# Kernel tuning notes

Hardware: AMD Instinct MI355X
Metric: run time of the kernel (lower is better)

Reference implementation:

```python
import jax, jax.numpy as jnp
import numpy as np

D_IN = 1024
D_OUT = 1024
NUM_HEADS = 16
HEAD_DIM = D_OUT // NUM_HEADS


def setup_inputs() -> dict:
    key = jax.random.key(0)
    kx, kq, kk, kv, ko = jax.random.split(key, 5)
    s = 1.0 / np.sqrt(D_IN)
    return {
        "x": jax.random.normal(kx, (1, 4096, D_IN), dtype=jnp.float32),
        "Wq": jax.random.normal(kq, (D_IN, D_OUT), dtype=jnp.float32) * s,
        "Wk": jax.random.normal(kk, (D_IN, D_OUT), dtype=jnp.float32) * s,
        "Wv": jax.random.normal(kv, (D_IN, D_OUT), dtype=jnp.float32) * s,
        "Wo": jax.random.normal(ko, (D_OUT, D_OUT), dtype=jnp.float32) * s,
    }


def reference(x, Wq, Wk, Wv, Wo):
    b, s, _ = x.shape
    # project and split heads: [b, h, s, d]
    def split_heads(t):
        return t.reshape(b, s, NUM_HEADS, HEAD_DIM).transpose(0, 2, 1, 3)
    Q = split_heads(x @ Wq)
    K = split_heads(x @ Wk)
    V = split_heads(x @ Wv)
    scores = jnp.einsum("bhqd,bhkd->bhqk", Q, K) / jnp.sqrt(jnp.float32(HEAD_DIM))
    causal = jnp.triu(jnp.ones((s, s), dtype=bool), k=1)  # True above diagonal
    scores = jnp.where(causal, -jnp.inf, scores)
    probs = jax.nn.softmax(scores, axis=-1)
    out = jnp.einsum("bhqk,bhkd->bhqd", probs, V)
    out = out.transpose(0, 2, 1, 3).reshape(b, s, D_OUT)
    return out @ Wo
```

## Files before the change

### kernel.cpp

```cpp
#include <hip/hip_runtime.h>
#include <cstdint>

#define S_LEN 4096
#define D_MODEL 1024
#define NHEAD 16
#define HDIM 64

typedef __bf16 bf16_t;
typedef __bf16 bf16x8 __attribute__((ext_vector_type(8)));
typedef __bf16 bf16x4 __attribute__((ext_vector_type(4)));
typedef float floatx4 __attribute__((ext_vector_type(4)));

#define QSCALE 0.18033688011112042f

__device__ __forceinline__ void lds_cp16(void* lds, const void* g) {
    __builtin_amdgcn_global_load_lds(
        (const __attribute__((address_space(1))) unsigned int*)g,
        (__attribute__((address_space(3))) unsigned int*)lds,
        16, 0, 0);
}

__global__ __launch_bounds__(256) void k_prep(const float* __restrict__ x,
                                              const float* __restrict__ Wq,
                                              const float* __restrict__ Wk,
                                              const float* __restrict__ Wv,
                                              const float* __restrict__ Wo,
                                              bf16_t* __restrict__ xb,
                                              bf16_t* __restrict__ WtQKV,
                                              bf16_t* __restrict__ WtO) {
    const int bx = blockIdx.x;
    if (bx < 4096) {
        int i = bx * 256 + threadIdx.x;
        float4 v = ((const float4*)x)[i];
        bf16x4 o;
        o[0] = (bf16_t)v.x; o[1] = (bf16_t)v.y; o[2] = (bf16_t)v.z; o[3] = (bf16_t)v.w;
        *(bf16x4*)(xb + (size_t)i * 4) = o;
        return;
    }
    __shared__ float lds[64][65];
    const int i = bx - 4096;
    const int z = i >> 8, rem = i & 255;
    const float* W = (z == 0) ? Wq : (z == 1) ? Wk : (z == 2) ? Wv : Wo;
    bf16_t* Wt = (z < 3) ? (WtQKV + (size_t)z * 1048576) : WtO;
    const int k0 = (rem >> 4) * 64, n0 = (rem & 15) * 64;
    const int t = threadIdx.x, cl = t & 63, rl = t >> 6;
#pragma unroll
    for (int r = 0; r < 16; ++r)
        lds[r * 4 + rl][cl] = W[(size_t)(k0 + r * 4 + rl) * 1024 + n0 + cl];
    __syncthreads();
#pragma unroll
    for (int r = 0; r < 16; ++r)
        Wt[(size_t)(n0 + r * 4 + rl) * 1024 + k0 + cl] = (bf16_t)lds[cl][r * 4 + rl];
}

template <int MODE>
__global__ __launch_bounds__(256) void k_gemm(const bf16_t* __restrict__ A,
                                              const bf16_t* __restrict__ Bt,
                                              float* __restrict__ Cout,
                                              bf16_t* __restrict__ Qb,
                                              bf16_t* __restrict__ Kb,
                                              bf16_t* __restrict__ Vt) {
    __shared__ __align__(16) bf16_t sA[128 * 32];
    __shared__ __align__(16) bf16_t sB[128 * 32];
    const int t = threadIdx.x, w = t >> 6, lane = t & 63, quad = lane >> 4, l15 = lane & 15;
    const int m0 = blockIdx.x * 128, n0 = blockIdx.y * 128;
    const int wm = w >> 1, wn = w & 1;

    floatx4 acc[4][4];
#pragma unroll
    for (int i = 0; i < 4; ++i)
#pragma unroll
        for (int j = 0; j < 4; ++j)
            acc[i][j] = floatx4{0.f, 0.f, 0.f, 0.f};

    for (int kb = 0; kb < 32; ++kb) {
        __syncthreads();
#pragma unroll
        for (int r = 0; r < 2; ++r) {
            int c = t + 256 * r;
            int row = c >> 2, kq = c & 3;
            lds_cp16(&sA[w * 512 + r * 2048],
                     A + (size_t)(m0 + row) * 1024 + kb * 32 + kq * 8);
            lds_cp16(&sB[w * 512 + r * 2048],
                     Bt + (size_t)(n0 + row) * 1024 + kb * 32 + kq * 8);
        }
        __syncthreads();
        bf16x8 af[4], bfr[4];
#pragma unroll
        for (int i = 0; i < 4; ++i)
            af[i] = *(const bf16x8*)&sA[(wm * 64 + i * 16 + l15) * 32 + quad * 8];
#pragma unroll
        for (int j = 0; j < 4; ++j)
            bfr[j] = *(const bf16x8*)&sB[(wn * 64 + j * 16 + l15) * 32 + quad * 8];
#pragma unroll
        for (int i = 0; i < 4; ++i)
#pragma unroll
            for (int j = 0; j < 4; ++j)
                acc[i][j] = __builtin_amdgcn_mfma_f32_16x16x32_bf16(af[i], bfr[j],
                                                                    acc[i][j], 0, 0, 0);
    }

    const int mrow = m0 + wm * 64 + quad * 4;
    if (MODE == 0) {
        const int ncol = n0 + wn * 64 + l15;
#pragma unroll
        for (int i = 0; i < 4; ++i)
#pragma unroll
            for (int j = 0; j < 4; ++j)
#pragma unroll
                for (int r = 0; r < 4; ++r)
                    Cout[(size_t)(mrow + i * 16 + r) * 1024 + ncol + j * 16] = acc[i][j][r];
    } else {
        const int g = (int)blockIdx.y >> 3;
        const int ncbase = ((int)blockIdx.y & 7) * 128 + wn * 64 + l15;
        if (g == 2) {
#pragma unroll
            for (int j = 0; j < 4; ++j) {
                int nc = ncbase + j * 16;
                int hh = nc >> 6, dd = nc & 63;
                bf16_t* dst = Vt + (size_t)hh * 262144 + (size_t)dd * 64;
#pragma unroll
                for (int i = 0; i < 4; ++i) {
                    int s0r = mrow + i * 16;
                    bf16x4 pk;
                    pk[0] = (bf16_t)acc[i][j][0]; pk[1] = (bf16_t)acc[i][j][1];
                    pk[2] = (bf16_t)acc[i][j][2]; pk[3] = (bf16_t)acc[i][j][3];
                    *(bf16x4*)&dst[(size_t)(s0r >> 6) * 4096 + (s0r & 63)] = pk;
                }
            }
        } else {
            bf16_t* base = g ? Kb : Qb;
            const float sc = g ? 1.0f : QSCALE;
#pragma unroll
            for (int j = 0; j < 4; ++j) {
                int nc = ncbase + j * 16;
                int hh = nc >> 6, dd = nc & 63;
#pragma unroll
                for (int i = 0; i < 4; ++i)
#pragma unroll
                    for (int r = 0; r < 4; ++r)
                        base[(size_t)hh * 262144 + (size_t)(mrow + i * 16 + r) * 64 + dd] =
                            (bf16_t)(acc[i][j][r] * sc);
            }
        }
    }
}

__global__ __launch_bounds__(256, 4) void k_attn(const bf16_t* __restrict__ Qb,
                                                 const bf16_t* __restrict__ Kb,
                                                 const bf16_t* __restrict__ Vt,
                                                 bf16_t* __restrict__ OP0,
                                                 bf16_t* __restrict__ OP1,
                                                 float* __restrict__ Lp) {
    __shared__ __align__(16) bf16_t Ks[2][64 * 64];
    __shared__ __align__(16) bf16_t Vts[64 * 64];
    __shared__ __align__(16) bf16_t Ps[4][32 * 64];
    const int bid = blockIdx.x;
    const int qb = 31 - (bid >> 5);
    const int sp = bid & 1, h = (bid & 31) >> 1;
    const int t = threadIdx.x, w = t >> 6, quad = (t & 63) >> 4, l15 = t & 15;
    const bf16_t* Qh = Qb + (size_t)h * 262144;
    const bf16_t* Kh = Kb + (size_t)h * 262144;
    const bf16_t* Vth = Vt + (size_t)h * 262144;
    bf16_t* PsW = &Ps[w][0];

    const bf16_t* Qrow = Qh + (size_t)(qb * 128 + w * 32 + l15) * 64;
    bf16x8 bq[2][2];
#pragma unroll
    for (int qt = 0; qt < 2; ++qt)
#pragma unroll
        for (int kh = 0; kh < 2; ++kh)
            bq[qt][kh] = *(const bf16x8*)(Qrow + qt * 1024 + kh * 32 + quad * 8);

    float l_s[2] = {0.f, 0.f};
    floatx4 o_acc[2][4];
#pragma unroll
    for (int qt = 0; qt < 2; ++qt)
#pragma unroll
        for (int j = 0; j < 4; ++j) o_acc[qt][j] = floatx4{0.f, 0.f, 0.f, 0.f};

#define STAGE_K(b, kb_)                                                            \
    {                                                                              \
        _Pragma("unroll") for (int r = 0; r < 2; ++r) {                            \
            int c = t + 256 * r;                                                   \
            int row = c >> 3, sw = (c & 7) ^ (row & 7);                            \
            lds_cp16(&Ks[b][c * 8], Kh + (size_t)(kb_) * 4096 + row * 64 + sw * 8);\
        }                                                                          \
    }
#define STAGE_V(kb_)                                                               \
    {                                                                              \
        _Pragma("unroll") for (int r = 0; r < 2; ++r) {                            \
            int c = t + 256 * r;                                                   \
            int row = c >> 3, sw = (c & 7) ^ (row & 7);                            \
            lds_cp16(&Vts[c * 8], Vth + (size_t)(kb_) * 4096 + row * 64 + sw * 8); \
        }                                                                          \
    }

    const int t0 = sp ? (qb + 1) : 0;
    const int nIter = qb + 1;
    const int qmax = qb * 128 + w * 32 + 31;

    STAGE_K(0, t0)
    for (int it = 0; it < nIter; ++it) {
        const int kb = t0 + it;
        const int buf = it & 1;
        __syncthreads();
        STAGE_V(kb)
        if (it + 1 < nIter) STAGE_K(buf ^ 1, kb + 1)
        const bool active = (kb * 64 <= qmax);

        if (active) {
            floatx4 st[2][4];
#pragma unroll
            for (int j = 0; j < 4; ++j) {
                int rk = j * 16 + l15;
                bf16x8 a0 = *(const bf16x8*)&Ks[buf][rk * 64 + ((quad ^ (rk & 7)) * 8)];
                bf16x8 a1 = *(const bf16x8*)&Ks[buf][rk * 64 + (((quad + 4) ^ (rk & 7)) * 8)];
#pragma unroll
                for (int qt = 0; qt < 2; ++qt) {
                    floatx4 z = {0.f, 0.f, 0.f, 0.f};
                    st[qt][j] = __builtin_amdgcn_mfma_f32_16x16x32_bf16(a0, bq[qt][0], z, 0, 0, 0);
                    st[qt][j] = __builtin_amdgcn_mfma_f32_16x16x32_bf16(a1, bq[qt][1], st[qt][j], 0, 0, 0);
                }
            }
            if (kb >= 2 * qb) {
#pragma unroll
                for (int qt = 0; qt < 2; ++qt) {
                    int qg = qb * 128 + w * 32 + qt * 16 + l15;
#pragma unroll
                    for (int j = 0; j < 4; ++j)
#pragma unroll
                        for (int r = 0; r < 4; ++r) {
                            int keyg = kb * 64 + j * 16 + quad * 4 + r;
                            if (keyg > qg) st[qt][j][r] = -1e30f;
                        }
                }
            }
#pragma unroll
            for (int qt = 0; qt < 2; ++qt) {
                float a0 = 0.f, a1 = 0.f, a2 = 0.f, a3 = 0.f;
#pragma unroll
                for (int j = 0; j < 4; ++j) {
                    float p0 = exp2f(st[qt][j][0]);
                    float p1 = exp2f(st[qt][j][1]);
                    float p2 = exp2f(st[qt][j][2]);
                    float p3 = exp2f(st[qt][j][3]);
                    a0 += p0; a1 += p1; a2 += p2; a3 += p3;
                    bf16x4 pk;
                    pk[0] = (bf16_t)p0; pk[1] = (bf16_t)p1;
                    pk[2] = (bf16_t)p2; pk[3] = (bf16_t)p3;
                    int c = j * 4 + quad;
                    *(bf16x4*)&PsW[(qt * 16 + l15) * 64 + (((c >> 1) ^ (l15 & 7)) * 8) +
                                   (c & 1) * 4] = pk;
                }
                l_s[qt] += (a0 + a1) + (a2 + a3);
            }
        }
        if (it + 1 < nIter) asm volatile("s_waitcnt vmcnt(2)" ::: "memory");
        else                asm volatile("s_waitcnt vmcnt(0)" ::: "memory");
        if (active) {
#pragma unroll
            for (int kh = 0; kh < 2; ++kh) {
                int pc = kh * 4 + quad;
                bf16x8 pa0 = *(const bf16x8*)&PsW[l15 * 64 + ((pc ^ (l15 & 7)) * 8)];
                bf16x8 pa1 = *(const bf16x8*)&PsW[(16 + l15) * 64 + ((pc ^ (l15 & 7)) * 8)];
#pragma unroll
                for (int j = 0; j < 4; ++j) {
                    int rd = j * 16 + l15;
                    bf16x8 bv = *(const bf16x8*)&Vts[rd * 64 + ((pc ^ (rd & 7)) * 8)];
                    o_acc[0][j] = __builtin_amdgcn_mfma_f32_16x16x32_bf16(pa0, bv, o_acc[0][j], 0, 0, 0);
                    o_acc[1][j] = __builtin_amdgcn_mfma_f32_16x16x32_bf16(pa1, bv, o_acc[1][j], 0, 0, 0);
                }
            }
        }
    }
    bf16_t* OPx = sp ? OP1 : OP0;
#pragma unroll
    for (int qt = 0; qt < 2; ++qt) {
        float l = l_s[qt];
        l += __shfl_xor(l, 16);
        l += __shfl_xor(l, 32);
        if (quad == 0)
            Lp[sp * 65536 + h * 4096 + (qb * 128 + w * 32 + qt * 16 + l15)] = l;
#pragma unroll
        for (int r = 0; r < 4; ++r) {
            int rowg = qb * 128 + w * 32 + qt * 16 + quad * 4 + r;
#pragma unroll
            for (int j = 0; j < 4; ++j)
                OPx[(size_t)rowg * 1024 + h * 64 + j * 16 + l15] = (bf16_t)o_acc[qt][j][r];
        }
    }
#undef STAGE_K
#undef STAGE_V
}

__global__ __launch_bounds__(256) void k_combine(const bf16_t* __restrict__ OP0,
                                                 const bf16_t* __restrict__ OP1,
                                                 const float* __restrict__ Lp,
                                                 bf16_t* __restrict__ Ob) {
    int gi = (blockIdx.x * 256 + threadIdx.x) * 4;
    int q = gi >> 10, hh = (gi & 1023) >> 6;
    float inv = 1.0f / (Lp[hh * 4096 + q] + Lp[65536 + hh * 4096 + q]);
    bf16x4 a = *(const bf16x4*)(OP0 + gi);
    bf16x4 b = *(const bf16x4*)(OP1 + gi);
    bf16x4 o;
#pragma unroll
    for (int r = 0; r < 4; ++r)
        o[r] = (bf16_t)(((float)a[r] + (float)b[r]) * inv);
    *(bf16x4*)(Ob + gi) = o;
}

extern "C" void kernel_launch(void* const* d_in, const int* in_sizes, int n_in,
                              void* d_out, int out_size, void* d_ws, size_t ws_size,
                              hipStream_t stream) {
    const float* x  = (const float*)d_in[0];
    const float* Wq = (const float*)d_in[1];
    const float* Wk = (const float*)d_in[2];
    const float* Wv = (const float*)d_in[3];
    const float* Wo = (const float*)d_in[4];

    bf16_t* ws = (bf16_t*)d_ws;
    bf16_t* Xb    = ws;
    bf16_t* WtQKV = Xb + 4194304;
    bf16_t* WtO   = WtQKV + 3145728;
    bf16_t* Qb    = WtO + 1048576;
    bf16_t* Kb    = Qb + 4194304;
    bf16_t* Vt    = Kb + 4194304;
    bf16_t* Ob    = Vt + 4194304;
    bf16_t* OP1   = Ob + 4194304;
    bf16_t* OP0   = Xb;
    float*  Lp    = (float*)WtQKV;
    float* out = (float*)d_out;

    k_prep<<<5120, 256, 0, stream>>>(x, Wq, Wk, Wv, Wo, Xb, WtQKV, WtO);
    k_gemm<1><<<dim3(32, 24), 256, 0, stream>>>(Xb, WtQKV, nullptr, Qb, Kb, Vt);
    k_attn<<<1024, 256, 0, stream>>>(Qb, Kb, Vt, OP0, OP1, Lp);
    k_combine<<<4096, 256, 0, stream>>>(OP0, OP1, Lp, Ob);
    k_gemm<0><<<dim3(32, 8), 256, 0, stream>>>(Ob, WtO, out, nullptr, nullptr, nullptr);
}
```

Measured before the change: 215.9 us.

## Keep softmax probabilities in registers via permuted V layout; rebalance attention block order

The V-transpose store now permutes key positions within each 64-key tile so that the MFMA output register layout of the score tile can be fed directly as the A operand of the PV MFMA. This removes the per-warp LDS staging buffer for P along with its writes and reads, and also reduces LDS usage. The block-index mapping is also changed to interleave long and short causal query blocks across dispatch slots for better load balance. The change relies on the permutation matching the MFMA lane layout exactly, and it adds register pressure from holding P.

Result: faster. 203.2 us (-5.9%).

```diff
diff --git a/kernel.cpp b/kernel.cpp
--- a/kernel.cpp
+++ b/kernel.cpp
@@ -125,7 +125,9 @@
                     bf16x4 pk;
                     pk[0] = (bf16_t)acc[i][j][0]; pk[1] = (bf16_t)acc[i][j][1];
                     pk[2] = (bf16_t)acc[i][j][2]; pk[3] = (bf16_t)acc[i][j][3];
-                    *(bf16x4*)&dst[(size_t)(s0r >> 6) * 4096 + (s0r & 63)] = pk;
+                    int kk = s0r & 63;
+                    int pp = (kk & 0x20) | ((kk & 0xC) << 1) | ((kk & 0x10) >> 2);
+                    *(bf16x4*)&dst[(size_t)(s0r >> 6) * 4096 + pp] = pk;
                 }
             }
         } else {
@@ -154,15 +156,15 @@
                                                  float* __restrict__ Lp) {
     __shared__ __align__(16) bf16_t Ks[2][64 * 64];
     __shared__ __align__(16) bf16_t Vts[64 * 64];
-    __shared__ __align__(16) bf16_t Ps[4][32 * 64];
     const int bid = blockIdx.x;
-    const int qb = 31 - (bid >> 5);
-    const int sp = bid & 1, h = (bid & 31) >> 1;
+    const int slot = bid >> 8, jj = bid & 255, g = jj >> 5, u = jj & 31;
+    const int h = u >> 1, sp = u & 1;
+    const int qb = (slot == 0) ? (31 - g) : (slot == 1) ? (16 + g)
+                 : (slot == 2) ? (15 - g) : g;
     const int t = threadIdx.x, w = t >> 6, quad = (t & 63) >> 4, l15 = t & 15;
     const bf16_t* Qh = Qb + (size_t)h * 262144;
     const bf16_t* Kh = Kb + (size_t)h * 262144;
     const bf16_t* Vth = Vt + (size_t)h * 262144;
-    bf16_t* PsW = &Ps[w][0];
 
     const bf16_t* Qrow = Qh + (size_t)(qb * 128 + w * 32 + l15) * 64;
     bf16x8 bq[2][2];
@@ -209,6 +211,7 @@
         if (it + 1 < nIter) STAGE_K(buf ^ 1, kb + 1)
         const bool active = (kb * 64 <= qmax);
 
+        bf16x8 pa[2][2];
         if (active) {
             floatx4 st[2][4];
 #pragma unroll
@@ -241,19 +244,19 @@
                 float a0 = 0.f, a1 = 0.f, a2 = 0.f, a3 = 0.f;
 #pragma unroll
                 for (int j = 0; j < 4; ++j) {
-                    float p0 = exp2f(st[qt][j][0]);
-                    float p1 = exp2f(st[qt][j][1]);
-                    float p2 = exp2f(st[qt][j][2]);
-                    float p3 = exp2f(st[qt][j][3]);
-                    a0 += p0; a1 += p1; a2 += p2; a3 += p3;
-                    bf16x4 pk;
-                    pk[0] = (bf16_t)p0; pk[1] = (bf16_t)p1;
-                    pk[2] = (bf16_t)p2; pk[3] = (bf16_t)p3;
-                    int c = j * 4 + quad;
-                    *(bf16x4*)&PsW[(qt * 16 + l15) * 64 + (((c >> 1) ^ (l15 & 7)) * 8) +
-                                   (c & 1) * 4] = pk;
+                    st[qt][j][0] = exp2f(st[qt][j][0]); a0 += st[qt][j][0];
+                    st[qt][j][1] = exp2f(st[qt][j][1]); a1 += st[qt][j][1];
+                    st[qt][j][2] = exp2f(st[qt][j][2]); a2 += st[qt][j][2];
+                    st[qt][j][3] = exp2f(st[qt][j][3]); a3 += st[qt][j][3];
                 }
                 l_s[qt] += (a0 + a1) + (a2 + a3);
+#pragma unroll
+                for (int kh = 0; kh < 2; ++kh)
+#pragma unroll
+                    for (int m = 0; m < 4; ++m) {
+                        pa[qt][kh][m]     = (bf16_t)st[qt][2 * kh][m];
+                        pa[qt][kh][4 + m] = (bf16_t)st[qt][2 * kh + 1][m];
+                    }
             }
         }
         if (it + 1 < nIter) asm volatile("s_waitcnt vmcnt(2)" ::: "memory");
@@ -262,14 +265,12 @@
 #pragma unroll
             for (int kh = 0; kh < 2; ++kh) {
                 int pc = kh * 4 + quad;
-                bf16x8 pa0 = *(const bf16x8*)&PsW[l15 * 64 + ((pc ^ (l15 & 7)) * 8)];
-                bf16x8 pa1 = *(const bf16x8*)&PsW[(16 + l15) * 64 + ((pc ^ (l15 & 7)) * 8)];
 #pragma unroll
                 for (int j = 0; j < 4; ++j) {
                     int rd = j * 16 + l15;
                     bf16x8 bv = *(const bf16x8*)&Vts[rd * 64 + ((pc ^ (rd & 7)) * 8)];
-                    o_acc[0][j] = __builtin_amdgcn_mfma_f32_16x16x32_bf16(pa0, bv, o_acc[0][j], 0, 0, 0);
-                    o_acc[1][j] = __builtin_amdgcn_mfma_f32_16x16x32_bf16(pa1, bv, o_acc[1][j], 0, 0, 0);
+                    o_acc[0][j] = __builtin_amdgcn_mfma_f32_16x16x32_bf16(pa[0][kh], bv, o_acc[0][j], 0, 0, 0);
+                    o_acc[1][j] = __builtin_amdgcn_mfma_f32_16x16x32_bf16(pa[1][kh], bv, o_acc[1][j], 0, 0, 0);
                 }
             }
         }
```
